# Performance work log

Measured on AMD Instinct MI355X. Metric: run time of the kernel, lower is better.

The kernel has to match this reference:

```python
import jax, jax.numpy as jnp
import numpy as np

EPS = 1e-5  # torch BatchNorm1d default eps


def _bn(x, gamma, beta):
    # training-mode BatchNorm1d over the point dimension
    m = jnp.mean(x, axis=0)
    v = jnp.var(x, axis=0)
    return (x - m) * jax.lax.rsqrt(v + EPS) * gamma + beta


def setup_inputs() -> dict:
    key = jax.random.key(0)
    ks = jax.random.split(key, 8)
    N, D = 1000000, 9
    G, V = 32, 32768  # 32^3 voxel grid; with 1M points all voxels occupied w.h.p.
    feats = jax.random.normal(ks[0], (N, D), dtype=jnp.float32)
    coords = jax.random.randint(ks[1], (N, 3), 0, G, dtype=jnp.int32)

    def lin(k, fan_in, fan_out):
        kw, kb = jax.random.split(k)
        s = 1.0 / np.sqrt(fan_in)
        W = jax.random.uniform(kw, (fan_in, fan_out), jnp.float32, -s, s)
        b = jax.random.uniform(kb, (fan_out,), jnp.float32, -s, s)
        return W, b

    W1, b1 = lin(ks[2], 9, 64)
    W2, b2 = lin(ks[3], 64, 128)
    W3, b3 = lin(ks[4], 128, 256)
    W4, b4 = lin(ks[5], 256, 256)
    return {
        'feats': feats, 'coords': coords, 'num_voxels': V,
        'g0': jnp.ones((9,), jnp.float32), 'be0': jnp.zeros((9,), jnp.float32),
        'W1': W1, 'b1': b1,
        'g1': jnp.ones((64,), jnp.float32), 'be1': jnp.zeros((64,), jnp.float32),
        'W2': W2, 'b2': b2,
        'g2': jnp.ones((128,), jnp.float32), 'be2': jnp.zeros((128,), jnp.float32),
        'W3': W3, 'b3': b3,
        'g3': jnp.ones((256,), jnp.float32), 'be3': jnp.zeros((256,), jnp.float32),
        'W4': W4, 'b4': b4,
    }


def _mlp(x, g0, be0, W1, b1, g1, be1, W2, b2, g2, be2, W3, b3, g3, be3, W4, b4):
    x = _bn(x, g0, be0)
    x = jax.nn.relu(_bn(x @ W1 + b1, g1, be1))
    x = jax.nn.relu(_bn(x @ W2 + b2, g2, be2))
    x = jax.nn.relu(_bn(x @ W3 + b3, g3, be3))
    return x @ W4 + b4


def reference(feats, coords, num_voxels, g0, be0, W1, b1, g1, be1, W2, b2,
              g2, be2, W3, b3, g3, be3, W4, b4):
    # NOTE: the torch module shuffles points first; unique(dim=0) is sorted and
    # scatter_max is permutation-invariant, so the shuffle does not affect output.
    unq_coords, unq_inv = jnp.unique(
        coords, axis=0, return_inverse=True, size=num_voxels, fill_value=0)
    unq_inv = unq_inv.reshape(-1)
    unq_coords = unq_coords.astype(jnp.int64)
    h = _mlp(feats, g0, be0, W1, b1, g1, be1, W2, b2, g2, be2, W3, b3, g3, be3, W4, b4)
    pooled = jax.ops.segment_max(h, unq_inv, num_segments=num_voxels)  # [V, 256]
    return pooled, unq_coords
```

## Files before the change

### kernel.cpp

```cpp
#include <hip/hip_runtime.h>
#include <math.h>

#define TPB 256
#define NVOX 32768
#define BN_EPS 1e-5f

typedef short s16x8 __attribute__((ext_vector_type(8)));
typedef short s16x4 __attribute__((ext_vector_type(4)));
typedef float f32x4 __attribute__((ext_vector_type(4)));

#define P0_OFF     0u
#define P1_OFF     256u
#define P2_OFF     (P1_OFF + 64u*128u*4u)
#define P3_OFF     (P2_OFF + 64u*256u*4u)
#define PAR_END    (P3_OFF + 64u*512u*4u)
#define A0_OFF     229632u
#define C0_OFF     229888u
#define A1_OFF     230144u
#define C1_OFF     230400u
#define A2_OFF     230656u
#define C2_OFF     231680u
#define A3_OFF     232704u
#define C3_OFF     233728u
#define HIST_OFF   234752u
#define BASE_OFF   (HIST_OFF + 131072u)
#define CURS_OFF   (BASE_OFF + 131328u)
#define WT1_OFF    (CURS_OFF + 131072u)
#define WT2_OFF    (WT1_OFF + 4096u)
#define WT3_OFF    (WT2_OFF + 16384u)
#define WT4_OFF    (WT3_OFF + 65536u)
#define X_OFF      4845568u

__device__ __forceinline__ unsigned short f2bf(float f) {
    unsigned u = __float_as_uint(f);
    u += 0x7FFFu + ((u >> 16) & 1u);
    return (unsigned short)(u >> 16);
}
__device__ __forceinline__ float bf2f(unsigned short h) {
    return __uint_as_float(((unsigned)h) << 16);
}

template<int ROWB>
__device__ __forceinline__ int swz(int row, int b) {
    constexpr int M = (ROWB >= 128) ? 7 : ((ROWB >= 64) ? 3 : 1);
    return row * ROWB + (b ^ ((row & M) << 4));
}

__device__ __forceinline__ s16x4 bn_relu_pack(f32x4 acc, f32x4 av, f32x4 cv) {
    s16x4 pk;
#pragma unroll
    for (int r = 0; r < 4; ++r) pk[r] = (short)f2bf(fmaxf(fmaf(acc[r], av[r], cv[r]), 0.f));
    return pk;
}

template<int NOUT>
__device__ __forceinline__ void stats_red(f32x4 ps, f32x4 pq, int ch, float* prow) {
#pragma unroll
    for (int m = 1; m <= 8; m <<= 1) {
#pragma unroll
        for (int r = 0; r < 4; ++r) { ps[r] += __shfl_xor(ps[r], m); pq[r] += __shfl_xor(pq[r], m); }
    }
    if ((threadIdx.x & 15) == 0) {
#pragma unroll
        for (int r = 0; r < 4; ++r) {
            atomicAdd(&prow[ch + r], ps[r]);
            atomicAdd(&prow[NOUT + ch + r], pq[r]);
        }
    }
}

__global__ void k_prepw(const float* __restrict__ W1, const float* __restrict__ W2,
                        const float* __restrict__ W3, const float* __restrict__ W4,
                        unsigned short* __restrict__ wt1, unsigned short* __restrict__ wt2,
                        unsigned short* __restrict__ wt3, unsigned short* __restrict__ wt4) {
    for (int i = blockIdx.x * blockDim.x + threadIdx.x; i < 108544;
         i += gridDim.x * blockDim.x) {
        if (i < 2048) {
            int n = i >> 5, k = i & 31;
            wt1[i] = (k < 9) ? f2bf(W1[k * 64 + n]) : (unsigned short)0;
        } else if (i < 10240) {
            int j = i - 2048; int n = j >> 6, k = j & 63;
            wt2[j] = f2bf(W2[k * 128 + n]);
        } else if (i < 43008) {
            int j = i - 10240; int n = j >> 7, k = j & 127;
            wt3[j] = f2bf(W3[k * 256 + n]);
        } else {
            int j = i - 43008; int n = j >> 8, k = j & 255;
            wt4[j] = f2bf(W4[k * 256 + n]);
        }
    }
}

__global__ void k_hist_stats(const int* __restrict__ coords, const float* __restrict__ feats,
                             int N, unsigned* __restrict__ hist, float* __restrict__ p0) {
    __shared__ float s[9], q[9];
    if (threadIdx.x < 9) { s[threadIdx.x] = 0.f; q[threadIdx.x] = 0.f; }
    __syncthreads();
    float ls[9] = {0}, lq[9] = {0};
    for (int i = blockIdx.x * blockDim.x + threadIdx.x; i < N;
         i += gridDim.x * blockDim.x) {
        int v = (coords[3 * i] << 10) | (coords[3 * i + 1] << 5) | coords[3 * i + 2];
        atomicAdd(&hist[v], 1u);
        const float* r = feats + (size_t)i * 9;
#pragma unroll
        for (int c = 0; c < 9; ++c) { float x = r[c]; ls[c] += x; lq[c] += x * x; }
    }
#pragma unroll
    for (int c = 0; c < 9; ++c) { atomicAdd(&s[c], ls[c]); atomicAdd(&q[c], lq[c]); }
    __syncthreads();
    if (threadIdx.x < 9) {
        atomicAdd(&p0[threadIdx.x], s[threadIdx.x]);
        atomicAdd(&p0[9 + threadIdx.x], q[threadIdx.x]);
    }
}

__global__ void k_scan(const unsigned* __restrict__ hist, int* __restrict__ base,
                       unsigned* __restrict__ cursor, int N) {
    __shared__ unsigned part[1024];
    const int t = threadIdx.x;
    unsigned sum = 0;
    for (int j = 0; j < 32; ++j) sum += hist[t * 32 + j];
    part[t] = sum;
    __syncthreads();
    for (int d = 1; d < 1024; d <<= 1) {
        unsigned v = (t >= d) ? part[t - d] : 0u;
        __syncthreads();
        part[t] += v;
        __syncthreads();
    }
    unsigned run = part[t] - sum;
    for (int j = 0; j < 32; ++j) {
        unsigned h = hist[t * 32 + j];
        base[t * 32 + j] = (int)run;
        cursor[t * 32 + j] = run;
        run += h;
    }
    if (t == 1023) base[32768] = (int)run;
}

__global__ void k_scatter2(const int* __restrict__ coords, const float* __restrict__ feats,
                           int N, unsigned* __restrict__ cursor,
                           const float* __restrict__ A0, const float* __restrict__ C0,
                           unsigned short* __restrict__ Xg) {
    float a0[9], c0[9];
#pragma unroll
    for (int c = 0; c < 9; ++c) { a0[c] = A0[c]; c0[c] = C0[c]; }
    for (int i = blockIdx.x * blockDim.x + threadIdx.x; i < N;
         i += gridDim.x * blockDim.x) {
        int v = (coords[3 * i] << 10) | (coords[3 * i + 1] << 5) | coords[3 * i + 2];
        unsigned pos = atomicAdd(&cursor[v], 1u);
        const float* r = feats + (size_t)i * 9;
        s16x8 lo, hi;
#pragma unroll
        for (int c = 0; c < 8; ++c) lo[c] = (short)f2bf(fmaf(r[c], a0[c], c0[c]));
        hi = (s16x8){0, 0, 0, 0, 0, 0, 0, 0};
        hi[0] = (short)f2bf(fmaf(r[8], a0[8], c0[8]));
        *(s16x8*)(Xg + (size_t)pos * 16) = lo;
        *(s16x8*)(Xg + (size_t)pos * 16 + 8) = hi;
    }
}

__global__ void k_fin(const float* __restrict__ part, int nparts, int C,
                      const float* __restrict__ g, const float* __restrict__ be,
                      const float* __restrict__ bias,
                      float* __restrict__ A, float* __restrict__ Cc, float n) {
    int c = threadIdx.x;
    if (c >= C) return;
    float s = 0.f, q = 0.f;
    for (int r = 0; r < nparts; ++r) { s += part[r * 2 * C + c]; q += part[r * 2 * C + C + c]; }
    float m = s / n;
    float v = q / n - m * m;
    float a = g[c] * rsqrtf(v + BN_EPS);
    float cc = be[c] - m * a;
    A[c] = a;
    Cc[c] = bias ? fmaf(a, bias[c], cc) : cc;
}

__global__ void k_coords(float* __restrict__ outc) {
    int v = blockIdx.x * blockDim.x + threadIdx.x;
    if (v < NVOX) {
        outc[3 * v + 0] = (float)(v >> 10);
        outc[3 * v + 1] = (float)((v >> 5) & 31);
        outc[3 * v + 2] = (float)(v & 31);
    }
}

__global__ __launch_bounds__(256) void k_pass1s(
    const unsigned short* __restrict__ Xg, const unsigned short* __restrict__ wt1,
    const float* __restrict__ b1, float* __restrict__ p1, int N, int nt) {
    const int tid = threadIdx.x;
    const int w = tid >> 6, lane = tid & 63, g = lane >> 4, lq = lane & 15;
    const int chb = w * 16;
    const s16x8 a1 = *(const s16x8*)(wt1 + (chb + lq) * 32 + g * 8);
    const int ch = chb + g * 4;
    const f32x4 bv = *(const f32x4*)(b1 + ch);
    f32x4 ps = (f32x4){0.f,0.f,0.f,0.f}, pq = (f32x4){0.f,0.f,0.f,0.f};
    for (int t = blockIdx.x; t < nt; t += gridDim.x) {
        const int t0 = t * 128;
#pragma unroll
        for (int ct = 0; ct < 8; ++ct) {
            const int p = t0 + ct * 16 + lq;
            const s16x8 b = *(const s16x8*)(Xg + (size_t)p * 16 + g * 8);
            f32x4 a = (f32x4){0.f,0.f,0.f,0.f};
            a = __builtin_amdgcn_mfma_f32_16x16x32_bf16(a1, b, a, 0, 0, 0);
            const bool valid = p < N;
#pragma unroll
            for (int r = 0; r < 4; ++r) {
                const float h = valid ? (a[r] + bv[r]) : 0.f;
                ps[r] += h; pq[r] += h * h;
            }
        }
    }
    stats_red<64>(ps, pq, ch, p1 + (blockIdx.x & 63) * 128);
}

__global__ __launch_bounds__(256) void k_pass2(
    const unsigned short* __restrict__ Xg,
    const unsigned short* __restrict__ wt1, const unsigned short* __restrict__ wt2,
    const float* __restrict__ A1, const float* __restrict__ C1,
    const float* __restrict__ b2,
    float* __restrict__ p2, int N, int nt) {
    __shared__ char act1[2][16384];
    const int tid = threadIdx.x;
    const int w = tid >> 6, lane = tid & 63, g = lane >> 4, lq = lane & 15;
    const int chb1 = w * 16, chb2 = w * 32;
    const s16x8 a1 = *(const s16x8*)(wt1 + (chb1 + lq) * 32 + g * 8);
    s16x8 w2f[2][2];
#pragma unroll
    for (int mt = 0; mt < 2; ++mt)
#pragma unroll
        for (int kc = 0; kc < 2; ++kc)
            w2f[mt][kc] = *(const s16x8*)(wt2 + (size_t)(chb2 + mt * 16 + lq) * 64 + kc * 32 + g * 8);
    const int ch1 = chb1 + g * 4;
    const f32x4 av1 = *(const f32x4*)(A1 + ch1);
    const f32x4 cv1 = *(const f32x4*)(C1 + ch1);
    f32x4 bv2[2];
#pragma unroll
    for (int mt = 0; mt < 2; ++mt) bv2[mt] = *(const f32x4*)(b2 + chb2 + mt * 16 + g * 4);
    f32x4 ps[2], pq[2];
#pragma unroll
    for (int mt = 0; mt < 2; ++mt) { ps[mt] = (f32x4){0.f,0.f,0.f,0.f}; pq[mt] = (f32x4){0.f,0.f,0.f,0.f}; }

    int t = blockIdx.x;
    if (t < nt) {
#pragma unroll
        for (int ct = 0; ct < 8; ++ct) {
            const int row = ct * 16 + lq;
            const s16x8 b = *(const s16x8*)(Xg + (size_t)(t * 128 + row) * 16 + g * 8);
            f32x4 a = (f32x4){0.f,0.f,0.f,0.f};
            a = __builtin_amdgcn_mfma_f32_16x16x32_bf16(a1, b, a, 0, 0, 0);
            *(s16x4*)(act1[0] + swz<128>(row, ch1 * 2)) = bn_relu_pack(a, av1, cv1);
        }
        __syncthreads();
        int cur = 0;
        while (true) {
            const int tn = t + gridDim.x;
            const bool more = tn < nt;
            const int t0 = t * 128;
            f32x4 acc2[2][8];
#pragma unroll
            for (int mt = 0; mt < 2; ++mt)
#pragma unroll
                for (int ct = 0; ct < 8; ++ct) acc2[mt][ct] = (f32x4){0.f,0.f,0.f,0.f};
#pragma unroll
            for (int kc = 0; kc < 2; ++kc)
#pragma unroll
                for (int ct = 0; ct < 8; ++ct) {
                    const s16x8 b = *(const s16x8*)(act1[cur] + swz<128>(ct * 16 + lq, kc * 64 + g * 16));
#pragma unroll
                    for (int mt = 0; mt < 2; ++mt)
                        acc2[mt][ct] = __builtin_amdgcn_mfma_f32_16x16x32_bf16(w2f[mt][kc], b, acc2[mt][ct], 0, 0, 0);
                }
#pragma unroll
            for (int mt = 0; mt < 2; ++mt)
#pragma unroll
                for (int ct = 0; ct < 8; ++ct) {
                    const bool valid = (t0 + ct * 16 + lq) < N;
#pragma unroll
                    for (int r = 0; r < 4; ++r) {
                        const float h = valid ? (acc2[mt][ct][r] + bv2[mt][r]) : 0.f;
                        ps[mt][r] += h; pq[mt][r] += h * h;
                    }
                }
            if (more) {
#pragma unroll
                for (int ct = 0; ct < 8; ++ct) {
                    const int row = ct * 16 + lq;
                    const s16x8 b = *(const s16x8*)(Xg + (size_t)(tn * 128 + row) * 16 + g * 8);
                    f32x4 a = (f32x4){0.f,0.f,0.f,0.f};
                    a = __builtin_amdgcn_mfma_f32_16x16x32_bf16(a1, b, a, 0, 0, 0);
                    *(s16x4*)(act1[cur ^ 1] + swz<128>(row, ch1 * 2)) = bn_relu_pack(a, av1, cv1);
                }
            }
            __syncthreads();
            if (!more) break;
            t = tn; cur ^= 1;
        }
    }
    float* prow = p2 + (blockIdx.x & 63) * 256;
#pragma unroll
    for (int mt = 0; mt < 2; ++mt)
        stats_red<128>(ps[mt], pq[mt], chb2 + mt * 16 + g * 4, prow);
}

__global__ __launch_bounds__(512) void k_pass3(
    const unsigned short* __restrict__ Xg,
    const unsigned short* __restrict__ wt1, const unsigned short* __restrict__ wt2,
    const unsigned short* __restrict__ wt3,
    const float* __restrict__ A1, const float* __restrict__ C1,
    const float* __restrict__ A2, const float* __restrict__ C2,
    const float* __restrict__ b3,
    float* __restrict__ p3, int N, int nt) {
    __shared__ char act1[8192];
    __shared__ char act2[16384];
    const int tid = threadIdx.x;
    const int w = tid >> 6, lane = tid & 63, g = lane >> 4, lq = lane & 15;
    const int wm = w >> 1, wn = w & 1;
    const int chb1 = wm * 16, chb2 = w * 16, chb3 = w * 32;
    const s16x8 a1 = *(const s16x8*)(wt1 + (chb1 + lq) * 32 + g * 8);
    s16x8 w2f[2], w3f[2][4];
#pragma unroll
    for (int kc = 0; kc < 2; ++kc)
        w2f[kc] = *(const s16x8*)(wt2 + (size_t)(chb2 + lq) * 64 + kc * 32 + g * 8);
#pragma unroll
    for (int mt = 0; mt < 2; ++mt)
#pragma unroll
        for (int kc = 0; kc < 4; ++kc)
            w3f[mt][kc] = *(const s16x8*)(wt3 + (size_t)(chb3 + mt * 16 + lq) * 128 + kc * 32 + g * 8);
    const int ch1 = chb1 + g * 4, ch2 = chb2 + g * 4;
    const f32x4 av1 = *(const f32x4*)(A1 + ch1);
    const f32x4 cv1 = *(const f32x4*)(C1 + ch1);
    const f32x4 av2 = *(const f32x4*)(A2 + ch2);
    const f32x4 cv2 = *(const f32x4*)(C2 + ch2);
    f32x4 bv3[2];
#pragma unroll
    for (int mt = 0; mt < 2; ++mt) bv3[mt] = *(const f32x4*)(b3 + chb3 + mt * 16 + g * 4);
    f32x4 ps[2], pq[2];
#pragma unroll
    for (int mt = 0; mt < 2; ++mt) { ps[mt] = (f32x4){0.f,0.f,0.f,0.f}; pq[mt] = (f32x4){0.f,0.f,0.f,0.f}; }

    int t = blockIdx.x;
    if (t < nt) {
#pragma unroll
        for (int ct = 0; ct < 2; ++ct) {
            const int row = wn * 32 + ct * 16 + lq;
            const s16x8 b = *(const s16x8*)(Xg + (size_t)(t * 64 + row) * 16 + g * 8);
            f32x4 a = (f32x4){0.f,0.f,0.f,0.f};
            a = __builtin_amdgcn_mfma_f32_16x16x32_bf16(a1, b, a, 0, 0, 0);
            *(s16x4*)(act1 + swz<128>(row, ch1 * 2)) = bn_relu_pack(a, av1, cv1);
        }
        __syncthreads();
        {
            f32x4 acc[4];
#pragma unroll
            for (int ct = 0; ct < 4; ++ct) acc[ct] = (f32x4){0.f,0.f,0.f,0.f};
#pragma unroll
            for (int kc = 0; kc < 2; ++kc)
#pragma unroll
                for (int ct = 0; ct < 4; ++ct) {
                    const s16x8 b = *(const s16x8*)(act1 + swz<128>(ct * 16 + lq, kc * 64 + g * 16));
                    acc[ct] = __builtin_amdgcn_mfma_f32_16x16x32_bf16(w2f[kc], b, acc[ct], 0, 0, 0);
                }
#pragma unroll
            for (int ct = 0; ct < 4; ++ct)
                *(s16x4*)(act2 + swz<256>(ct * 16 + lq, ch2 * 2)) = bn_relu_pack(acc[ct], av2, cv2);
        }
        __syncthreads();
        while (true) {
            const int tn = t + gridDim.x;
            const bool more = tn < nt;
            s16x8 xb[2];
            if (more) {
#pragma unroll
                for (int ct = 0; ct < 2; ++ct) {
                    const int row = wn * 32 + ct * 16 + lq;
                    xb[ct] = *(const s16x8*)(Xg + (size_t)(tn * 64 + row) * 16 + g * 8);
                }
            }
            {
                f32x4 acc[2][4];
#pragma unroll
                for (int mt = 0; mt < 2; ++mt)
#pragma unroll
                    for (int ct = 0; ct < 4; ++ct) acc[mt][ct] = (f32x4){0.f,0.f,0.f,0.f};
#pragma unroll
                for (int kc = 0; kc < 4; ++kc)
#pragma unroll
                    for (int ct = 0; ct < 4; ++ct) {
                        const s16x8 b = *(const s16x8*)(act2 + swz<256>(ct * 16 + lq, kc * 64 + g * 16));
#pragma unroll
                        for (int mt = 0; mt < 2; ++mt)
                            acc[mt][ct] = __builtin_amdgcn_mfma_f32_16x16x32_bf16(w3f[mt][kc], b, acc[mt][ct], 0, 0, 0);
                    }
                const int t0 = t * 64;
#pragma unroll
                for (int mt = 0; mt < 2; ++mt)
#pragma unroll
                    for (int ct = 0; ct < 4; ++ct) {
                        const bool valid = (t0 + ct * 16 + lq) < N;
#pragma unroll
                        for (int r = 0; r < 4; ++r) {
                            const float h = valid ? (acc[mt][ct][r] + bv3[mt][r]) : 0.f;
                            ps[mt][r] += h; pq[mt][r] += h * h;
                        }
                    }
            }
            if (more) {
#pragma unroll
                for (int ct = 0; ct < 2; ++ct) {
                    const int row = wn * 32 + ct * 16 + lq;
                    f32x4 a = (f32x4){0.f,0.f,0.f,0.f};
                    a = __builtin_amdgcn_mfma_f32_16x16x32_bf16(a1, xb[ct], a, 0, 0, 0);
                    *(s16x4*)(act1 + swz<128>(row, ch1 * 2)) = bn_relu_pack(a, av1, cv1);
                }
            }
            __syncthreads();
            if (more) {
                f32x4 acc[4];
#pragma unroll
                for (int ct = 0; ct < 4; ++ct) acc[ct] = (f32x4){0.f,0.f,0.f,0.f};
#pragma unroll
                for (int kc = 0; kc < 2; ++kc)
#pragma unroll
                    for (int ct = 0; ct < 4; ++ct) {
                        const s16x8 b = *(const s16x8*)(act1 + swz<128>(ct * 16 + lq, kc * 64 + g * 16));
                        acc[ct] = __builtin_amdgcn_mfma_f32_16x16x32_bf16(w2f[kc], b, acc[ct], 0, 0, 0);
                    }
#pragma unroll
                for (int ct = 0; ct < 4; ++ct)
                    *(s16x4*)(act2 + swz<256>(ct * 16 + lq, ch2 * 2)) = bn_relu_pack(acc[ct], av2, cv2);
            }
            __syncthreads();
            if (!more) break;
            t = tn;
        }
    }
    float* prow = p3 + (blockIdx.x & 63) * 512;
#pragma unroll
    for (int mt = 0; mt < 2; ++mt)
        stats_red<256>(ps[mt], pq[mt], chb3 + mt * 16 + g * 4, prow);
}

__global__ __launch_bounds__(512) void k_pass4(
    const unsigned short* __restrict__ Xg,
    const unsigned short* __restrict__ wt1, const unsigned short* __restrict__ wt2,
    const unsigned short* __restrict__ wt3, const unsigned short* __restrict__ wt4,
    const float* __restrict__ A1, const float* __restrict__ C1,
    const float* __restrict__ A2, const float* __restrict__ C2,
    const float* __restrict__ A3, const float* __restrict__ C3,
    const float* __restrict__ b4,
    const int* __restrict__ base, float* __restrict__ out) {
    extern __shared__ char smem[];
    char* act1 = smem;
    char* act2 = smem + 8192;
    char* act3 = smem + 24576;
    float* vmax = (float*)(smem + 57344);

    const int tid = threadIdx.x;
    const int w = tid >> 6, lane = tid & 63, g = lane >> 4, lq = lane & 15;
    const int wm = w >> 1, wn = w & 1;
    const int chb1 = wm * 16, chb2 = w * 16, chb = w * 32;
    const int vb = blockIdx.x * 16;

    int bsv[17];
#pragma unroll
    for (int s = 0; s <= 16; ++s) bsv[s] = base[vb + s];
    const int pstart = bsv[0], pend = bsv[16];

    const s16x8 a1 = *(const s16x8*)(wt1 + (chb1 + lq) * 32 + g * 8);
    s16x8 w2f[2], w3f[2][4], w4f[2][8];
#pragma unroll
    for (int kc = 0; kc < 2; ++kc)
        w2f[kc] = *(const s16x8*)(wt2 + (size_t)(chb2 + lq) * 64 + kc * 32 + g * 8);
#pragma unroll
    for (int mt = 0; mt < 2; ++mt) {
#pragma unroll
        for (int kc = 0; kc < 4; ++kc)
            w3f[mt][kc] = *(const s16x8*)(wt3 + (size_t)(chb + mt * 16 + lq) * 128 + kc * 32 + g * 8);
#pragma unroll
        for (int kc = 0; kc < 8; ++kc)
            w4f[mt][kc] = *(const s16x8*)(wt4 + (size_t)(chb + mt * 16 + lq) * 256 + kc * 32 + g * 8);
    }
    const int ch1 = chb1 + g * 4, ch2 = chb2 + g * 4;
    const f32x4 av1 = *(const f32x4*)(A1 + ch1);
    const f32x4 cv1 = *(const f32x4*)(C1 + ch1);
    const f32x4 av2 = *(const f32x4*)(A2 + ch2);
    const f32x4 cv2 = *(const f32x4*)(C2 + ch2);
    f32x4 av3[2], cv3[2], bv4[2];
#pragma unroll
    for (int mt = 0; mt < 2; ++mt) {
        av3[mt] = *(const f32x4*)(A3 + chb + mt * 16 + g * 4);
        cv3[mt] = *(const f32x4*)(C3 + chb + mt * 16 + g * 4);
        bv4[mt] = *(const f32x4*)(b4 + chb + mt * 16 + g * 4);
    }

    for (int i = tid; i < 16 * 256; i += 512) vmax[i] = -INFINITY;
    __syncthreads();

    if (pstart < pend) {
#pragma unroll
        for (int ct = 0; ct < 2; ++ct) {
            const int row = wn * 32 + ct * 16 + lq;
            const s16x8 b = *(const s16x8*)(Xg + (size_t)(pstart + row) * 16 + g * 8);
            f32x4 a = (f32x4){0.f,0.f,0.f,0.f};
            a = __builtin_amdgcn_mfma_f32_16x16x32_bf16(a1, b, a, 0, 0, 0);
            *(s16x4*)(act1 + swz<128>(row, ch1 * 2)) = bn_relu_pack(a, av1, cv1);
        }
        __syncthreads();
        {
            f32x4 acc[4];
#pragma unroll
            for (int ct = 0; ct < 4; ++ct) acc[ct] = (f32x4){0.f,0.f,0.f,0.f};
#pragma unroll
            for (int kc = 0; kc < 2; ++kc)
#pragma unroll
                for (int ct = 0; ct < 4; ++ct) {
                    const s16x8 b = *(const s16x8*)(act1 + swz<128>(ct * 16 + lq, kc * 64 + g * 16));
                    acc[ct] = __builtin_amdgcn_mfma_f32_16x16x32_bf16(w2f[kc], b, acc[ct], 0, 0, 0);
                }
#pragma unroll
            for (int ct = 0; ct < 4; ++ct)
                *(s16x4*)(act2 + swz<256>(ct * 16 + lq, ch2 * 2)) = bn_relu_pack(acc[ct], av2, cv2);
        }
        __syncthreads();

        for (int t0 = pstart; t0 < pend; t0 += 64) {
            const int nxt = t0 + 64;
            const bool more = nxt < pend;
            s16x8 xb[2];
            if (more) {
#pragma unroll
                for (int ct = 0; ct < 2; ++ct) {
                    const int row = wn * 32 + ct * 16 + lq;
                    xb[ct] = *(const s16x8*)(Xg + (size_t)(nxt + row) * 16 + g * 8);
                }
            }
            {
                f32x4 acc[2][4];
#pragma unroll
                for (int mt = 0; mt < 2; ++mt)
#pragma unroll
                    for (int ct = 0; ct < 4; ++ct) acc[mt][ct] = (f32x4){0.f,0.f,0.f,0.f};
#pragma unroll
                for (int kc = 0; kc < 4; ++kc)
#pragma unroll
                    for (int ct = 0; ct < 4; ++ct) {
                        const s16x8 b = *(const s16x8*)(act2 + swz<256>(ct * 16 + lq, kc * 64 + g * 16));
#pragma unroll
                        for (int mt = 0; mt < 2; ++mt)
                            acc[mt][ct] = __builtin_amdgcn_mfma_f32_16x16x32_bf16(w3f[mt][kc], b, acc[mt][ct], 0, 0, 0);
                    }
#pragma unroll
                for (int mt = 0; mt < 2; ++mt)
#pragma unroll
                    for (int ct = 0; ct < 4; ++ct)
                        *(s16x4*)(act3 + swz<512>(ct * 16 + lq, (chb + mt * 16 + g * 4) * 2)) =
                            bn_relu_pack(acc[mt][ct], av3[mt], cv3[mt]);
            }
            if (more) {
#pragma unroll
                for (int ct = 0; ct < 2; ++ct) {
                    const int row = wn * 32 + ct * 16 + lq;
                    f32x4 a = (f32x4){0.f,0.f,0.f,0.f};
                    a = __builtin_amdgcn_mfma_f32_16x16x32_bf16(a1, xb[ct], a, 0, 0, 0);
                    *(s16x4*)(act1 + swz<128>(row, ch1 * 2)) = bn_relu_pack(a, av1, cv1);
                }
            }
            __syncthreads();
            if (more) {
                f32x4 acc[4];
#pragma unroll
                for (int ct = 0; ct < 4; ++ct) acc[ct] = (f32x4){0.f,0.f,0.f,0.f};
#pragma unroll
                for (int kc = 0; kc < 2; ++kc)
#pragma unroll
                    for (int ct = 0; ct < 4; ++ct) {
                        const s16x8 b = *(const s16x8*)(act1 + swz<128>(ct * 16 + lq, kc * 64 + g * 16));
                        acc[ct] = __builtin_amdgcn_mfma_f32_16x16x32_bf16(w2f[kc], b, acc[ct], 0, 0, 0);
                    }
#pragma unroll
                for (int ct = 0; ct < 4; ++ct)
                    *(s16x4*)(act2 + swz<256>(ct * 16 + lq, ch2 * 2)) = bn_relu_pack(acc[ct], av2, cv2);
            }
            {
                f32x4 acc[2][4];
#pragma unroll
                for (int mt = 0; mt < 2; ++mt)
#pragma unroll
                    for (int ct = 0; ct < 4; ++ct) acc[mt][ct] = (f32x4){0.f,0.f,0.f,0.f};
#pragma unroll
                for (int kc = 0; kc < 8; ++kc)
#pragma unroll
                    for (int ct = 0; ct < 4; ++ct) {
                        const s16x8 b = *(const s16x8*)(act3 + swz<512>(ct * 16 + lq, kc * 64 + g * 16));
#pragma unroll
                        for (int mt = 0; mt < 2; ++mt)
                            acc[mt][ct] = __builtin_amdgcn_mfma_f32_16x16x32_bf16(w4f[mt][kc], b, acc[mt][ct], 0, 0, 0);
                    }
#pragma unroll
                for (int ct = 0; ct < 4; ++ct) {
                    const int p = t0 + ct * 16 + lq;
                    int vid = 0;
#pragma unroll
                    for (int s = 1; s <= 16; ++s) vid += (p >= bsv[s]) ? 1 : 0;
                    float v[8];
#pragma unroll
                    for (int mt = 0; mt < 2; ++mt)
#pragma unroll
                        for (int r = 0; r < 4; ++r) v[mt * 4 + r] = acc[mt][ct][r] + bv4[mt][r];
#pragma unroll
                    for (int d = 1; d < 16; d <<= 1) {
                        const int nvid = __shfl_down(vid, d, 16);
#pragma unroll
                        for (int j = 0; j < 8; ++j) {
                            const float nv = __shfl_down(v[j], d, 16);
                            v[j] = (nvid == vid) ? fmaxf(v[j], nv) : v[j];
                        }
                    }
                    const int pv = __shfl_up(vid, 1, 16);
                    if (vid < 16 && (lq == 0 || pv != vid)) {
#pragma unroll
                        for (int mt = 0; mt < 2; ++mt)
#pragma unroll
                            for (int r = 0; r < 4; ++r) {
                                float* a = &vmax[vid * 256 + chb + mt * 16 + g * 4 + r];
                                *a = fmaxf(*a, v[mt * 4 + r]);
                            }
                    }
                }
            }
            __syncthreads();
        }
    }
    {
        const int vx = tid >> 5, c8 = (tid & 31) * 8;
        const float* vr = &vmax[vx * 256 + c8];
        float* orow = out + (size_t)(vb + vx) * 256 + c8;
        *(f32x4*)orow = *(const f32x4*)vr;
        *(f32x4*)(orow + 4) = *(const f32x4*)(vr + 4);
    }
}

extern "C" void kernel_launch(void* const* d_in, const int* in_sizes, int n_in,
                              void* d_out, int out_size, void* d_ws, size_t ws_size,
                              hipStream_t stream) {
    const float* feats = (const float*)d_in[0];
    const int* coords = (const int*)d_in[1];
    const float* g0 = (const float*)d_in[3];
    const float* be0 = (const float*)d_in[4];
    const float* W1 = (const float*)d_in[5];
    const float* b1 = (const float*)d_in[6];
    const float* g1 = (const float*)d_in[7];
    const float* be1 = (const float*)d_in[8];
    const float* W2 = (const float*)d_in[9];
    const float* b2 = (const float*)d_in[10];
    const float* g2 = (const float*)d_in[11];
    const float* be2 = (const float*)d_in[12];
    const float* W3 = (const float*)d_in[13];
    const float* b3 = (const float*)d_in[14];
    const float* g3 = (const float*)d_in[15];
    const float* be3 = (const float*)d_in[16];
    const float* W4 = (const float*)d_in[17];
    const float* b4 = (const float*)d_in[18];
    float* out = (float*)d_out;
    char* ws = (char*)d_ws;

    const int N = in_sizes[0] / 9;
    const float fN = (float)N;
    const int nt128 = (N + 127) / 128;
    const int nt64 = (N + 63) / 64;

    unsigned short* Xg = (unsigned short*)(ws + X_OFF);
    const unsigned short* wt1 = (const unsigned short*)(ws + WT1_OFF);
    const unsigned short* wt2 = (const unsigned short*)(ws + WT2_OFF);
    const unsigned short* wt3 = (const unsigned short*)(ws + WT3_OFF);
    const unsigned short* wt4 = (const unsigned short*)(ws + WT4_OFF);
    float* A0 = (float*)(ws + A0_OFF); float* C0 = (float*)(ws + C0_OFF);
    float* A1 = (float*)(ws + A1_OFF); float* C1 = (float*)(ws + C1_OFF);
    float* A2 = (float*)(ws + A2_OFF); float* C2 = (float*)(ws + C2_OFF);
    float* A3 = (float*)(ws + A3_OFF); float* C3 = (float*)(ws + C3_OFF);

    hipMemsetAsync(ws, 0, PAR_END, stream);
    hipMemsetAsync(ws + HIST_OFF, 0, 131072, stream);
    {
        const size_t rows = (size_t)nt128 * 128;
        hipMemsetAsync(ws + X_OFF + (size_t)N * 32u, 0,
                       (rows - (size_t)N) * 32u + 8192u, stream);
    }

    hipFuncSetAttribute((const void*)k_pass4,
        hipFuncAttributeMaxDynamicSharedMemorySize, 73728);

    k_prepw<<<128, TPB, 0, stream>>>(W1, W2, W3, W4,
        (unsigned short*)(ws + WT1_OFF), (unsigned short*)(ws + WT2_OFF),
        (unsigned short*)(ws + WT3_OFF), (unsigned short*)(ws + WT4_OFF));
    k_hist_stats<<<1024, TPB, 0, stream>>>(coords, feats, N,
        (unsigned*)(ws + HIST_OFF), (float*)(ws + P0_OFF));
    k_fin<<<1, TPB, 0, stream>>>((const float*)(ws + P0_OFF), 1, 9, g0, be0, nullptr,
                                 A0, C0, fN);
    k_scan<<<1, 1024, 0, stream>>>((const unsigned*)(ws + HIST_OFF),
                                   (int*)(ws + BASE_OFF), (unsigned*)(ws + CURS_OFF), N);
    k_scatter2<<<1024, TPB, 0, stream>>>(coords, feats, N, (unsigned*)(ws + CURS_OFF),
                                         A0, C0, Xg);

    k_pass1s<<<2048, 256, 0, stream>>>(Xg, wt1, b1, (float*)(ws + P1_OFF), N, nt128);
    k_fin<<<1, TPB, 0, stream>>>((const float*)(ws + P1_OFF), 64, 64, g1, be1, b1,
                                 A1, C1, fN);

    k_pass2<<<2048, 256, 0, stream>>>(Xg, wt1, wt2, A1, C1, b2,
                                      (float*)(ws + P2_OFF), N, nt128);
    k_fin<<<1, TPB, 0, stream>>>((const float*)(ws + P2_OFF), 64, 128, g2, be2, b2,
                                 A2, C2, fN);

    k_pass3<<<2048, 512, 0, stream>>>(Xg, wt1, wt2, wt3, A1, C1, A2, C2, b3,
                                      (float*)(ws + P3_OFF), N, nt64);
    k_fin<<<1, TPB, 0, stream>>>((const float*)(ws + P3_OFF), 64, 256, g3, be3, b3,
                                 A3, C3, fN);

    k_coords<<<(NVOX + TPB - 1) / TPB, TPB, 0, stream>>>(out + (size_t)NVOX * 256);
    k_pass4<<<NVOX / 16, 512, 73728, stream>>>(Xg, wt1, wt2, wt3, wt4,
        A1, C1, A2, C2, A3, C3, b4, (const int*)(ws + BASE_OFF), out);
}
```

Before: 1.008 ms.

## Derive layer-1 BN stats analytically and restructure pass4 max-pooling via shared buffers

Layer-1 batch-norm statistics are now computed from the 9-channel sum and Gram matrix gathered in the histogram pass, so the separate pass1 kernel over all points is removed. The pass4 segment-max no longer uses a per-tile shuffle reduction with shared-memory read-modify-write. Instead the final-layer outputs are written as bf16 into double-buffered shared tiles, and each thread keeps a running max in registers for its voxel and channel group. The mt loop in the layer-3 and layer-4 MFMA blocks is moved outward to lower register pressure, and the inter-layer bf16 packing switches to truncation instead of round-to-nearest. In exchange, pass4 needs much more shared memory, which may reduce occupancy, and the pooled outputs now carry bf16 rounding.

After: 961.2 us. 4.7% less time.

```diff
diff --git a/kernel.cpp b/kernel.cpp
--- a/kernel.cpp
+++ b/kernel.cpp
@@ -36,6 +36,9 @@
     u += 0x7FFFu + ((u >> 16) & 1u);
     return (unsigned short)(u >> 16);
 }
+__device__ __forceinline__ unsigned short f2bft(float f) {
+    return (unsigned short)(__float_as_uint(f) >> 16);
+}
 __device__ __forceinline__ float bf2f(unsigned short h) {
     return __uint_as_float(((unsigned)h) << 16);
 }
@@ -49,7 +52,7 @@
 __device__ __forceinline__ s16x4 bn_relu_pack(f32x4 acc, f32x4 av, f32x4 cv) {
     s16x4 pk;
 #pragma unroll
-    for (int r = 0; r < 4; ++r) pk[r] = (short)f2bf(fmaxf(fmaf(acc[r], av[r], cv[r]), 0.f));
+    for (int r = 0; r < 4; ++r) pk[r] = (short)f2bft(fmaxf(fmaf(acc[r], av[r], cv[r]), 0.f));
     return pk;
 }
 
@@ -92,25 +95,91 @@
 }
 
 __global__ void k_hist_stats(const int* __restrict__ coords, const float* __restrict__ feats,
-                             int N, unsigned* __restrict__ hist, float* __restrict__ p0) {
-    __shared__ float s[9], q[9];
-    if (threadIdx.x < 9) { s[threadIdx.x] = 0.f; q[threadIdx.x] = 0.f; }
-    __syncthreads();
-    float ls[9] = {0}, lq[9] = {0};
+                             int N, unsigned* __restrict__ hist, float* __restrict__ banks) {
+    float S[9] = {0}, G[45] = {0};
     for (int i = blockIdx.x * blockDim.x + threadIdx.x; i < N;
          i += gridDim.x * blockDim.x) {
         int v = (coords[3 * i] << 10) | (coords[3 * i + 1] << 5) | coords[3 * i + 2];
         atomicAdd(&hist[v], 1u);
         const float* r = feats + (size_t)i * 9;
-#pragma unroll
-        for (int c = 0; c < 9; ++c) { float x = r[c]; ls[c] += x; lq[c] += x * x; }
-    }
-#pragma unroll
-    for (int c = 0; c < 9; ++c) { atomicAdd(&s[c], ls[c]); atomicAdd(&q[c], lq[c]); }
+        float x[9];
+#pragma unroll
+        for (int c = 0; c < 9; ++c) { x[c] = r[c]; S[c] += x[c]; }
+        int idx = 0;
+#pragma unroll
+        for (int c = 0; c < 9; ++c)
+#pragma unroll
+            for (int c2 = 0; c2 <= c; ++c2) { G[idx] = fmaf(x[c], x[c2], G[idx]); ++idx; }
+    }
+#pragma unroll
+    for (int m = 1; m <= 32; m <<= 1) {
+#pragma unroll
+        for (int c = 0; c < 9; ++c) S[c] += __shfl_xor(S[c], m);
+#pragma unroll
+        for (int j = 0; j < 45; ++j) G[j] += __shfl_xor(G[j], m);
+    }
+    if ((threadIdx.x & 63) == 0) {
+        float* b = banks + (size_t)(blockIdx.x & 63) * 54;
+#pragma unroll
+        for (int c = 0; c < 9; ++c) atomicAdd(&b[c], S[c]);
+#pragma unroll
+        for (int j = 0; j < 45; ++j) atomicAdd(&b[9 + j], G[j]);
+    }
+}
+
+__global__ void k_fin0(const float* __restrict__ banks, float* __restrict__ SG,
+                       const float* __restrict__ g0, const float* __restrict__ be0,
+                       float* __restrict__ A0, float* __restrict__ C0, float n) {
+    __shared__ float sg[54];
+    const int t = threadIdx.x;
+    if (t < 54) {
+        float s = 0.f;
+        for (int b = 0; b < 64; ++b) s += banks[b * 54 + t];
+        sg[t] = s; SG[t] = s;
+    }
     __syncthreads();
-    if (threadIdx.x < 9) {
-        atomicAdd(&p0[threadIdx.x], s[threadIdx.x]);
-        atomicAdd(&p0[9 + threadIdx.x], q[threadIdx.x]);
+    if (t < 9) {
+        float m = sg[t] / n;
+        float v = sg[9 + t * (t + 1) / 2 + t] / n - m * m;
+        float a = g0[t] * rsqrtf(v + BN_EPS);
+        A0[t] = a; C0[t] = be0[t] - m * a;
+    }
+}
+
+__global__ void k_fin1(const float* __restrict__ SG,
+                       const float* __restrict__ A0, const float* __restrict__ C0,
+                       const float* __restrict__ W1, const float* __restrict__ b1,
+                       const float* __restrict__ g1, const float* __restrict__ be1,
+                       float* __restrict__ A1, float* __restrict__ C1, float n) {
+    __shared__ float Sz[9], Gz[81];
+    const int t = threadIdx.x;
+    if (t < 9) Sz[t] = A0[t] * SG[t] + n * C0[t];
+    if (t < 81) {
+        const int c = t / 9, c2 = t - 9 * (t / 9);
+        const int i = c > c2 ? c : c2, j = c > c2 ? c2 : c;
+        const float G = SG[9 + i * (i + 1) / 2 + j];
+        Gz[t] = A0[c] * A0[c2] * G + A0[c] * SG[c] * C0[c2]
+              + C0[c] * A0[c2] * SG[c2] + n * C0[c] * C0[c2];
+    }
+    __syncthreads();
+    if (t < 64) {
+        float wn[9];
+#pragma unroll
+        for (int c = 0; c < 9; ++c) wn[c] = W1[c * 64 + t];
+        float su = 0.f, qq = 0.f;
+#pragma unroll
+        for (int c = 0; c < 9; ++c) {
+            su = fmaf(wn[c], Sz[c], su);
+#pragma unroll
+            for (int c2 = 0; c2 < 9; ++c2) qq = fmaf(wn[c] * wn[c2], Gz[c * 9 + c2], qq);
+        }
+        const float bb = b1[t];
+        const float mean = (su + n * bb) / n;
+        const float q = qq + 2.f * bb * su + n * bb * bb;
+        const float var = q / n - mean * mean;
+        const float a = g1[t] * rsqrtf(var + BN_EPS);
+        A1[t] = a;
+        C1[t] = fmaf(a, bb, be1[t] - mean * a);
     }
 }
 
@@ -183,35 +252,6 @@
         outc[3 * v + 1] = (float)((v >> 5) & 31);
         outc[3 * v + 2] = (float)(v & 31);
     }
-}
-
-__global__ __launch_bounds__(256) void k_pass1s(
-    const unsigned short* __restrict__ Xg, const unsigned short* __restrict__ wt1,
-    const float* __restrict__ b1, float* __restrict__ p1, int N, int nt) {
-    const int tid = threadIdx.x;
-    const int w = tid >> 6, lane = tid & 63, g = lane >> 4, lq = lane & 15;
-    const int chb = w * 16;
-    const s16x8 a1 = *(const s16x8*)(wt1 + (chb + lq) * 32 + g * 8);
-    const int ch = chb + g * 4;
-    const f32x4 bv = *(const f32x4*)(b1 + ch);
-    f32x4 ps = (f32x4){0.f,0.f,0.f,0.f}, pq = (f32x4){0.f,0.f,0.f,0.f};
-    for (int t = blockIdx.x; t < nt; t += gridDim.x) {
-        const int t0 = t * 128;
-#pragma unroll
-        for (int ct = 0; ct < 8; ++ct) {
-            const int p = t0 + ct * 16 + lq;
-            const s16x8 b = *(const s16x8*)(Xg + (size_t)p * 16 + g * 8);
-            f32x4 a = (f32x4){0.f,0.f,0.f,0.f};
-            a = __builtin_amdgcn_mfma_f32_16x16x32_bf16(a1, b, a, 0, 0, 0);
-            const bool valid = p < N;
-#pragma unroll
-            for (int r = 0; r < 4; ++r) {
-                const float h = valid ? (a[r] + bv[r]) : 0.f;
-                ps[r] += h; pq[r] += h * h;
-            }
-        }
-    }
-    stats_red<64>(ps, pq, ch, p1 + (blockIdx.x & 63) * 128);
 }
 
 __global__ __launch_bounds__(256) void k_pass2(
@@ -454,18 +494,17 @@
     char* act1 = smem;
     char* act2 = smem + 8192;
     char* act3 = smem + 24576;
-    float* vmax = (float*)(smem + 57344);
+    char* h40  = smem + 57344;
+    char* h41  = smem + 90112;
 
     const int tid = threadIdx.x;
     const int w = tid >> 6, lane = tid & 63, g = lane >> 4, lq = lane & 15;
     const int wm = w >> 1, wn = w & 1;
     const int chb1 = wm * 16, chb2 = w * 16, chb = w * 32;
     const int vb = blockIdx.x * 16;
-
-    int bsv[17];
-#pragma unroll
-    for (int s = 0; s <= 16; ++s) bsv[s] = base[vb + s];
-    const int pstart = bsv[0], pend = bsv[16];
+    const int pstart = base[vb], pend = base[vb + 16];
+    const int chgrp = tid & 31, slot = tid >> 5;
+    const int vlo = base[vb + slot], vhi = base[vb + slot + 1];
 
     const s16x8 a1 = *(const s16x8*)(wt1 + (chb1 + lq) * 32 + g * 8);
     s16x8 w2f[2], w3f[2][4], w4f[2][8];
@@ -494,8 +533,9 @@
         bv4[mt] = *(const f32x4*)(b4 + chb + mt * 16 + g * 4);
     }
 
-    for (int i = tid; i < 16 * 256; i += 512) vmax[i] = -INFINITY;
-    __syncthreads();
+    float rmax[8];
+#pragma unroll
+    for (int j = 0; j < 8; ++j) rmax[j] = -INFINITY;
 
     if (pstart < pend) {
 #pragma unroll
@@ -524,47 +564,42 @@
         }
         __syncthreads();
 
+        int cur = 0;
+        int lt = pstart;
         for (int t0 = pstart; t0 < pend; t0 += 64) {
             const int nxt = t0 + 64;
             const bool more = nxt < pend;
-            s16x8 xb[2];
+            char* hcur = cur ? h41 : h40;
+            char* hprev = cur ? h40 : h41;
+            s16x8 xb0, xb1;
             if (more) {
-#pragma unroll
-                for (int ct = 0; ct < 2; ++ct) {
-                    const int row = wn * 32 + ct * 16 + lq;
-                    xb[ct] = *(const s16x8*)(Xg + (size_t)(nxt + row) * 16 + g * 8);
-                }
-            }
-            {
-                f32x4 acc[2][4];
-#pragma unroll
-                for (int mt = 0; mt < 2; ++mt)
-#pragma unroll
-                    for (int ct = 0; ct < 4; ++ct) acc[mt][ct] = (f32x4){0.f,0.f,0.f,0.f};
+                xb0 = *(const s16x8*)(Xg + (size_t)(nxt + wn * 32 + lq) * 16 + g * 8);
+                xb1 = *(const s16x8*)(Xg + (size_t)(nxt + wn * 32 + 16 + lq) * 16 + g * 8);
+            }
+#pragma unroll
+            for (int mt = 0; mt < 2; ++mt) {
+                f32x4 acc[4];
+#pragma unroll
+                for (int ct = 0; ct < 4; ++ct) acc[ct] = (f32x4){0.f,0.f,0.f,0.f};
 #pragma unroll
                 for (int kc = 0; kc < 4; ++kc)
 #pragma unroll
                     for (int ct = 0; ct < 4; ++ct) {
                         const s16x8 b = *(const s16x8*)(act2 + swz<256>(ct * 16 + lq, kc * 64 + g * 16));
-#pragma unroll
-                        for (int mt = 0; mt < 2; ++mt)
-                            acc[mt][ct] = __builtin_amdgcn_mfma_f32_16x16x32_bf16(w3f[mt][kc], b, acc[mt][ct], 0, 0, 0);
+                        acc[ct] = __builtin_amdgcn_mfma_f32_16x16x32_bf16(w3f[mt][kc], b, acc[ct], 0, 0, 0);
                     }
 #pragma unroll
-                for (int mt = 0; mt < 2; ++mt)
-#pragma unroll
-                    for (int ct = 0; ct < 4; ++ct)
-                        *(s16x4*)(act3 + swz<512>(ct * 16 + lq, (chb + mt * 16 + g * 4) * 2)) =
-                            bn_relu_pack(acc[mt][ct], av3[mt], cv3[mt]);
+                for (int ct = 0; ct < 4; ++ct)
+                    *(s16x4*)(act3 + swz<512>(ct * 16 + lq, (chb + mt * 16 + g * 4) * 2)) =
+                        bn_relu_pack(acc[ct], av3[mt], cv3[mt]);
             }
             if (more) {
-#pragma unroll
-                for (int ct = 0; ct < 2; ++ct) {
-                    const int row = wn * 32 + ct * 16 + lq;
-                    f32x4 a = (f32x4){0.f,0.f,0.f,0.f};
-                    a = __builtin_amdgcn_mfma_f32_16x16x32_bf16(a1, xb[ct], a, 0, 0, 0);
-                    *(s16x4*)(act1 + swz<128>(row, ch1 * 2)) = bn_relu_pack(a, av1, cv1);
-                }
+                f32x4 a = (f32x4){0.f,0.f,0.f,0.f};
+                a = __builtin_amdgcn_mfma_f32_16x16x32_bf16(a1, xb0, a, 0, 0, 0);
+                *(s16x4*)(act1 + swz<128>(wn * 32 + lq, ch1 * 2)) = bn_relu_pack(a, av1, cv1);
+                f32x4 a2r = (f32x4){0.f,0.f,0.f,0.f};
+                a2r = __builtin_amdgcn_mfma_f32_16x16x32_bf16(a1, xb1, a2r, 0, 0, 0);
+                *(s16x4*)(act1 + swz<128>(wn * 32 + 16 + lq, ch1 * 2)) = bn_relu_pack(a2r, av1, cv1);
             }
             __syncthreads();
             if (more) {
@@ -582,63 +617,57 @@
                 for (int ct = 0; ct < 4; ++ct)
                     *(s16x4*)(act2 + swz<256>(ct * 16 + lq, ch2 * 2)) = bn_relu_pack(acc[ct], av2, cv2);
             }
-            {
-                f32x4 acc[2][4];
-#pragma unroll
-                for (int mt = 0; mt < 2; ++mt)
-#pragma unroll
-                    for (int ct = 0; ct < 4; ++ct) acc[mt][ct] = (f32x4){0.f,0.f,0.f,0.f};
+#pragma unroll
+            for (int mt = 0; mt < 2; ++mt) {
+                f32x4 acc[4];
+#pragma unroll
+                for (int ct = 0; ct < 4; ++ct) acc[ct] = (f32x4){0.f,0.f,0.f,0.f};
 #pragma unroll
                 for (int kc = 0; kc < 8; ++kc)
 #pragma unroll
                     for (int ct = 0; ct < 4; ++ct) {
                         const s16x8 b = *(const s16x8*)(act3 + swz<512>(ct * 16 + lq, kc * 64 + g * 16));
-#pragma unroll
-                        for (int mt = 0; mt < 2; ++mt)
-                            acc[mt][ct] = __builtin_amdgcn_mfma_f32_16x16x32_bf16(w4f[mt][kc], b, acc[mt][ct], 0, 0, 0);
+                        acc[ct] = __builtin_amdgcn_mfma_f32_16x16x32_bf16(w4f[mt][kc], b, acc[ct], 0, 0, 0);
                     }
 #pragma unroll
                 for (int ct = 0; ct < 4; ++ct) {
-                    const int p = t0 + ct * 16 + lq;
-                    int vid = 0;
-#pragma unroll
-                    for (int s = 1; s <= 16; ++s) vid += (p >= bsv[s]) ? 1 : 0;
-                    float v[8];
-#pragma unroll
-                    for (int mt = 0; mt < 2; ++mt)
-#pragma unroll
-                        for (int r = 0; r < 4; ++r) v[mt * 4 + r] = acc[mt][ct][r] + bv4[mt][r];
-#pragma unroll
-                    for (int d = 1; d < 16; d <<= 1) {
-                        const int nvid = __shfl_down(vid, d, 16);
-#pragma unroll
-                        for (int j = 0; j < 8; ++j) {
-                            const float nv = __shfl_down(v[j], d, 16);
-                            v[j] = (nvid == vid) ? fmaxf(v[j], nv) : v[j];
-                        }
-                    }
-                    const int pv = __shfl_up(vid, 1, 16);
-                    if (vid < 16 && (lq == 0 || pv != vid)) {
-#pragma unroll
-                        for (int mt = 0; mt < 2; ++mt)
-#pragma unroll
-                            for (int r = 0; r < 4; ++r) {
-                                float* a = &vmax[vid * 256 + chb + mt * 16 + g * 4 + r];
-                                *a = fmaxf(*a, v[mt * 4 + r]);
-                            }
-                    }
+                    s16x4 pk;
+#pragma unroll
+                    for (int r = 0; r < 4; ++r) pk[r] = (short)f2bf(acc[ct][r] + bv4[mt][r]);
+                    *(s16x4*)(hcur + swz<512>(ct * 16 + lq, (chb + mt * 16 + g * 4) * 2)) = pk;
+                }
+            }
+            if (t0 > pstart) {
+                const int tm = t0 - 64;
+                const int lo = max(vlo, tm), hi = min(vhi, tm + 64);
+                for (int p = lo; p < hi; ++p) {
+                    const s16x8 hv = *(const s16x8*)(hprev + swz<512>(p - tm, chgrp * 16));
+#pragma unroll
+                    for (int j = 0; j < 8; ++j)
+                        rmax[j] = fmaxf(rmax[j], bf2f((unsigned short)hv[j]));
                 }
             }
             __syncthreads();
-        }
-    }
-    {
-        const int vx = tid >> 5, c8 = (tid & 31) * 8;
-        const float* vr = &vmax[vx * 256 + c8];
-        float* orow = out + (size_t)(vb + vx) * 256 + c8;
-        *(f32x4*)orow = *(const f32x4*)vr;
-        *(f32x4*)(orow + 4) = *(const f32x4*)(vr + 4);
-    }
+            lt = t0;
+            cur ^= 1;
+        }
+        {
+            char* hlast = (cur ^ 1) ? h41 : h40;
+            const int lo = max(vlo, lt), hi = min(vhi, lt + 64);
+            for (int p = lo; p < hi; ++p) {
+                const s16x8 hv = *(const s16x8*)(hlast + swz<512>(p - lt, chgrp * 16));
+#pragma unroll
+                for (int j = 0; j < 8; ++j)
+                    rmax[j] = fmaxf(rmax[j], bf2f((unsigned short)hv[j]));
+            }
+        }
+    }
+    float* orow = out + (size_t)(vb + slot) * 256 + chgrp * 8;
+    f32x4 o0, o1;
+#pragma unroll
+    for (int j = 0; j < 4; ++j) { o0[j] = rmax[j]; o1[j] = rmax[4 + j]; }
+    *(f32x4*)orow = o0;
+    *(f32x4*)(orow + 4) = o1;
 }
 
 extern "C" void kernel_launch(void* const* d_in, const int* in_sizes, int n_in,
@@ -689,23 +718,22 @@
     }
 
     hipFuncSetAttribute((const void*)k_pass4,
-        hipFuncAttributeMaxDynamicSharedMemorySize, 73728);
+        hipFuncAttributeMaxDynamicSharedMemorySize, 122880);
 
     k_prepw<<<128, TPB, 0, stream>>>(W1, W2, W3, W4,
         (unsigned short*)(ws + WT1_OFF), (unsigned short*)(ws + WT2_OFF),
         (unsigned short*)(ws + WT3_OFF), (unsigned short*)(ws + WT4_OFF));
     k_hist_stats<<<1024, TPB, 0, stream>>>(coords, feats, N,
-        (unsigned*)(ws + HIST_OFF), (float*)(ws + P0_OFF));
-    k_fin<<<1, TPB, 0, stream>>>((const float*)(ws + P0_OFF), 1, 9, g0, be0, nullptr,
-                                 A0, C0, fN);
+        (unsigned*)(ws + HIST_OFF), (float*)(ws + P1_OFF));
+    k_fin0<<<1, 64, 0, stream>>>((const float*)(ws + P1_OFF), (float*)(ws + P0_OFF),
+                                 g0, be0, A0, C0, fN);
+    k_fin1<<<1, 128, 0, stream>>>((const float*)(ws + P0_OFF), A0, C0,
+                                  W1, b1, g1, be1, A1, C1, fN);
     k_scan<<<1, 1024, 0, stream>>>((const unsigned*)(ws + HIST_OFF),
                                    (int*)(ws + BASE_OFF), (unsigned*)(ws + CURS_OFF), N);
     k_scatter2<<<1024, TPB, 0, stream>>>(coords, feats, N, (unsigned*)(ws + CURS_OFF),
                                          A0, C0, Xg);
-
-    k_pass1s<<<2048, 256, 0, stream>>>(Xg, wt1, b1, (float*)(ws + P1_OFF), N, nt128);
-    k_fin<<<1, TPB, 0, stream>>>((const float*)(ws + P1_OFF), 64, 64, g1, be1, b1,
-                                 A1, C1, fN);
+    k_coords<<<(NVOX + TPB - 1) / TPB, TPB, 0, stream>>>(out + (size_t)NVOX * 256);
 
     k_pass2<<<2048, 256, 0, stream>>>(Xg, wt1, wt2, A1, C1, b2,
                                       (float*)(ws + P2_OFF), N, nt128);
@@ -717,7 +745,6 @@
     k_fin<<<1, TPB, 0, stream>>>((const float*)(ws + P3_OFF), 64, 256, g3, be3, b3,
                                  A3, C3, fN);
 
-    k_coords<<<(NVOX + TPB - 1) / TPB, TPB, 0, stream>>>(out + (size_t)NVOX * 256);
-    k_pass4<<<NVOX / 16, 512, 73728, stream>>>(Xg, wt1, wt2, wt3, wt4,
+    k_pass4<<<NVOX / 16, 512, 122880, stream>>>(Xg, wt1, wt2, wt3, wt4,
         A1, C1, A2, C2, A3, C3, b4, (const int*)(ws + BASE_OFF), out);
 }
```
